# Performance work log

Hardware: AMD Instinct MI355X
Metric: run time of the kernel (lower is better)

Reference implementation:

```python
import jax, jax.numpy as jnp
import numpy as np
from jax import lax

SCORE_TH = 0.05
IOU_TH = 0.5
MAX_DET = 100  # fixed keep budget per class (torch version is variable-length; we pad)
BBOX_STD = jnp.array([0.1, 0.1, 0.2, 0.2], dtype=jnp.float32)


def setup_inputs() -> dict:
    key = jax.random.key(0)
    k1, k2, k3, k4 = jax.random.split(key, 4)
    A, C, H, W = 200000, 80, 768, 768
    # sigmoid-like scores, skewed low so the 0.05 threshold is meaningful
    classification = jax.random.uniform(k1, (A, C), dtype=jnp.float32) ** 4
    regression = jax.random.normal(k2, (A, 4), dtype=jnp.float32)
    ctr = jax.random.uniform(k3, (A, 2), dtype=jnp.float32, minval=0.0, maxval=float(W))
    wh = jax.random.uniform(k4, (A, 2), dtype=jnp.float32, minval=8.0, maxval=128.0)
    anchors = jnp.concatenate([ctr - 0.5 * wh, ctr + 0.5 * wh], axis=-1)  # valid x1y1x2y2
    return {"classification": classification, "regression": regression,
            "anchors": anchors, "img_h": H, "img_w": W}


def _decode_clip(anchors, regression, img_h, img_w):
    # BBoxTransform: RetinaNet delta decode with std [0.1,0.1,0.2,0.2], then ClipBoxes
    wa = anchors[:, 2] - anchors[:, 0]
    ha = anchors[:, 3] - anchors[:, 1]
    cxa = anchors[:, 0] + 0.5 * wa
    cya = anchors[:, 1] + 0.5 * ha
    d = regression * BBOX_STD
    cx = cxa + d[:, 0] * wa
    cy = cya + d[:, 1] * ha
    w = jnp.exp(d[:, 2]) * wa
    h = jnp.exp(d[:, 3]) * ha
    boxes = jnp.stack([cx - 0.5 * w, cy - 0.5 * h, cx + 0.5 * w, cy + 0.5 * h], axis=-1)
    lim = jnp.array([img_w, img_h, img_w, img_h], dtype=boxes.dtype)
    return jnp.clip(boxes, 0.0, lim)


def _nms_one(scores_c, boxes, areas):
    # greedy NMS for one class over all A anchors; fixed MAX_DET iterations
    s0 = jnp.where(scores_c > SCORE_TH, scores_c, -1.0)

    def step(s, _):
        i = jnp.argmax(s)
        valid = s[i] > 0.0
        b = boxes[i]
        xx1 = jnp.maximum(b[0], boxes[:, 0])
        yy1 = jnp.maximum(b[1], boxes[:, 1])
        xx2 = jnp.minimum(b[2], boxes[:, 2])
        yy2 = jnp.minimum(b[3], boxes[:, 3])
        inter = jnp.maximum(xx2 - xx1, 0.0) * jnp.maximum(yy2 - yy1, 0.0)
        iou = inter / (areas[i] + areas - inter)
        supp = (iou > IOU_TH) & valid
        s = jnp.where(supp, -1.0, s).at[i].set(-1.0)
        return s, (i, valid)

    _, (idx, val) = lax.scan(step, s0, None, length=MAX_DET)
    return idx, val  # [MAX_DET] int, [MAX_DET] bool


def _forward(classification, regression, anchors, img_h, img_w):
    boxes = _decode_clip(anchors, regression, img_h, img_w)  # [A,4]
    # NMS index selection is non-differentiable (as in torch); stop_gradient the selection path
    boxes_ng = lax.stop_gradient(boxes)
    scores_ng = lax.stop_gradient(classification)
    areas = (boxes_ng[:, 2] - boxes_ng[:, 0]) * (boxes_ng[:, 3] - boxes_ng[:, 1])
    idx, val = jax.vmap(_nms_one, in_axes=(1, None, None))(scores_ng, boxes_ng, areas)  # [C,M]
    C = classification.shape[1]
    sel_scores = jnp.take_along_axis(classification.T, idx, axis=1) * val          # [C,M]
    sel_boxes = boxes[idx] * val[..., None]                                        # [C,M,4]
    class_ids = jnp.where(val, jnp.arange(C, dtype=jnp.int32)[:, None], -1)        # [C,M]
    # torch returns variable-length concatenations; we return fixed-size padded
    # equivalents (invalid slots: score=0, class=-1, box=0)
    return sel_scores.reshape(-1), class_ids.reshape(-1), sel_boxes.reshape(-1, 4)


def reference(classification, regression, anchors, img_h, img_w):
    return _forward(classification, regression, anchors, img_h, img_w)
```

## Files before the change

### kernel.cpp

```cpp
#include <hip/hip_runtime.h>
#include <float.h>
#include <math.h>

#define SCORE_TH 0.05f
#define IOU_TH   0.5f
#define MAXD     100
#define CAP      512
#define HI_TH    0.996f
#define SWALK    192
#define NWORDS   3
#define CNT_STRIDE 16

__device__ __forceinline__ float4 decode_box(float4 an, float4 r, float W, float H)
{
    float wa = an.z - an.x, ha = an.w - an.y;
    float cxa = an.x + 0.5f * wa, cya = an.y + 0.5f * ha;
    float cx = cxa + r.x * 0.1f * wa;
    float cy = cya + r.y * 0.1f * ha;
    float w  = expf(r.z * 0.2f) * wa;
    float h  = expf(r.w * 0.2f) * ha;
    float x1 = cx - 0.5f * w, y1 = cy - 0.5f * h;
    float x2 = cx + 0.5f * w, y2 = cy + 0.5f * h;
    x1 = fminf(fmaxf(x1, 0.f), W);
    y1 = fminf(fmaxf(y1, 0.f), H);
    x2 = fminf(fmaxf(x2, 0.f), W);
    y2 = fminf(fmaxf(y2, 0.f), H);
    return make_float4(x1, y1, x2, y2);
}

template<int CC>
__global__ __launch_bounds__(256)
void k_compact(const float4* __restrict__ cls4, float2* __restrict__ cand,
               int* __restrict__ cnt, int* __restrict__ loflag,
               int C_rt, int total4)
{
    const int C = CC ? CC : C_rt;
    __shared__ unsigned char lflag[256];
    for (int i = threadIdx.x; i < C; i += blockDim.x) lflag[i] = 0;
    __syncthreads();

    const int gstride = gridDim.x * blockDim.x;
    const int gtid = blockIdx.x * blockDim.x + threadIdx.x;

    for (int j0 = gtid; j0 < total4; j0 += 4 * gstride) {
        int j1 = j0 + gstride, j2 = j0 + 2 * gstride, j3 = j0 + 3 * gstride;
        bool ok1 = j1 < total4, ok2 = j2 < total4, ok3 = j3 < total4;
        float4 v0 = cls4[j0];
        float4 v1 = ok1 ? cls4[j1] : make_float4(0.f, 0.f, 0.f, 0.f);
        float4 v2 = ok2 ? cls4[j2] : make_float4(0.f, 0.f, 0.f, 0.f);
        float4 v3 = ok3 ? cls4[j3] : make_float4(0.f, 0.f, 0.f, 0.f);

        #pragma unroll
        for (int w = 0; w < 4; w++) {
            float4 v = (w == 0) ? v0 : (w == 1) ? v1 : (w == 2) ? v2 : v3;
            if (w == 1 && !ok1) break;
            if (w == 2 && !ok2) break;
            if (w == 3 && !ok3) break;
            unsigned b = (unsigned)(j0 + w * gstride) * 4u;
            int c = (int)(b % (unsigned)C);
            int a = (int)(b / (unsigned)C);
            float s[4] = {v.x, v.y, v.z, v.w};
            #pragma unroll
            for (int j = 0; j < 4; j++) {
                float sc = s[j];
                if (sc > HI_TH) {
                    int pos = atomicAdd(&cnt[c * CNT_STRIDE], 1);
                    if (pos < CAP) cand[(size_t)c * CAP + pos] = make_float2(sc, __int_as_float(a));
                } else if (sc > SCORE_TH) {
                    lflag[c] = 1;
                }
                c++; if (c == C) { c = 0; a++; }
            }
        }
    }
    __syncthreads();
    for (int i = threadIdx.x; i < C; i += blockDim.x)
        if (lflag[i]) loflag[i] = 1;
}

__global__ __launch_bounds__(256)
void k_nms(const float4* __restrict__ anch, const float4* __restrict__ reg,
           const int* __restrict__ ph, const int* __restrict__ pw,
           const float2* __restrict__ cand, const int* __restrict__ cnt,
           const int* __restrict__ loflag, int* __restrict__ incomp,
           float* __restrict__ out, int C)
{
    int c = blockIdx.x;
    __shared__ unsigned long long keys[CAP];
    __shared__ float bx1[SWALK], by1[SWALK], bx2[SWALK], by2[SWALK], sar[SWALK];
    __shared__ unsigned long long mask[SWALK][NWORDS];
    __shared__ int kidx[MAXD];

    int n_raw = cnt[c * CNT_STRIDE];
    if (n_raw > CAP) {
        if (threadIdx.x == 0) incomp[c] = 1;
        return;
    }
    int n = n_raw;

    for (int i = threadIdx.x; i < CAP; i += blockDim.x) {
        if (i < n) {
            float2 e = cand[(size_t)c * CAP + i];
            unsigned sbits = __float_as_uint(e.x);
            unsigned aid   = (unsigned)__float_as_int(e.y);
            keys[i] = ((unsigned long long)(~sbits) << 32) | (unsigned long long)aid;
        } else {
            keys[i] = 0xFFFFFFFFFFFFFFFFull;
        }
    }
    __syncthreads();

    const int SORTN = (n <= 256) ? 256 : CAP;
    for (int k = 2; k <= SORTN; k <<= 1) {
        for (int j = k >> 1; j > 0; j >>= 1) {
            for (int i = threadIdx.x; i < SORTN; i += blockDim.x) {
                int ixj = i ^ j;
                if (ixj > i) {
                    unsigned long long a = keys[i], b = keys[ixj];
                    bool sw = ((i & k) == 0) ? (a > b) : (a < b);
                    if (sw) { keys[i] = b; keys[ixj] = a; }
                }
            }
            __syncthreads();
        }
    }

    float W = (float)(*pw), H = (float)(*ph);
    int nS = n < SWALK ? n : SWALK;
    for (int i = threadIdx.x; i < nS; i += blockDim.x) {
        unsigned aid = (unsigned)keys[i];
        float4 b = decode_box(anch[aid], reg[aid], W, H);
        bx1[i] = b.x; by1[i] = b.y; bx2[i] = b.z; by2[i] = b.w;
        sar[i] = (b.z - b.x) * (b.w - b.y);
    }
    __syncthreads();

    for (int task = threadIdx.x; task < nS * NWORDS; task += blockDim.x) {
        int i = task / NWORDS;
        int w = task - i * NWORDS;
        unsigned long long m = 0ull;
        int j0 = w << 6;
        int jend = j0 + 64 < nS ? j0 + 64 : nS;
        int js = j0 > i + 1 ? j0 : i + 1;
        float ix1 = bx1[i], iy1 = by1[i], ix2 = bx2[i], iy2 = by2[i], ia = sar[i];
        for (int j = js; j < jend; ++j) {
            float xx1 = fmaxf(ix1, bx1[j]);
            float yy1 = fmaxf(iy1, by1[j]);
            float xx2 = fminf(ix2, bx2[j]);
            float yy2 = fminf(iy2, by2[j]);
            float inter = fmaxf(xx2 - xx1, 0.f) * fmaxf(yy2 - yy1, 0.f);
            float iou = inter / (ia + sar[j] - inter);
            if (iou > IOU_TH) m |= 1ull << (j - j0);
        }
        mask[i][w] = m;
    }
    __syncthreads();

    unsigned long long rem0 = 0, rem1 = 0, rem2 = 0;
    int kept = 0;
    for (int k = 0; k < nS && kept < MAXD; ++k) {
        unsigned long long m0 = mask[k][0], m1 = mask[k][1], m2 = mask[k][2];
        unsigned long long rw = (k < 64) ? rem0 : (k < 128) ? rem1 : rem2;
        if (!((rw >> (k & 63)) & 1ull)) {
            if (threadIdx.x == 0) kidx[kept] = k;
            ++kept;
            rem0 |= m0; rem1 |= m1; rem2 |= m2;
        }
    }
    __syncthreads();

    if (kept < MAXD && (n > nS || loflag[c] != 0)) {
        if (threadIdx.x == 0) incomp[c] = 1;
        return;
    }

    int total = C * MAXD;
    int base = c * MAXD;
    for (int m = threadIdx.x; m < kept; m += blockDim.x) {
        int k = kidx[m];
        unsigned long long key = keys[k];
        float sc = __uint_as_float(~(unsigned)(key >> 32));
        out[base + m] = sc;
        out[total + base + m] = (float)c;
        float* ob = out + 2 * (size_t)total + (size_t)(base + m) * 4;
        ob[0] = bx1[k]; ob[1] = by1[k]; ob[2] = bx2[k]; ob[3] = by2[k];
    }
    for (int m = kept + threadIdx.x; m < MAXD; m += blockDim.x) {
        out[base + m] = 0.f;
        out[total + base + m] = -1.f;
        float* ob = out + 2 * (size_t)total + (size_t)(base + m) * 4;
        ob[0] = 0.f; ob[1] = 0.f; ob[2] = 0.f; ob[3] = 0.f;
    }
}

__global__ __launch_bounds__(256)
void k_fallback(const float* __restrict__ cls,
                const float4* __restrict__ anch, const float4* __restrict__ reg,
                const int* __restrict__ ph, const int* __restrict__ pw,
                const int* __restrict__ incomp, float* __restrict__ out,
                int A, int C)
{
    int c = blockIdx.x;
    if (!incomp[c]) return;
    __shared__ float kx1[MAXD], ky1[MAXD], kx2[MAXD], ky2[MAXD], kar[MAXD];
    __shared__ float rs[4]; __shared__ int ra[4];
    __shared__ float cs; __shared__ int caid; __shared__ int have; __shared__ int suppflag;
    int lane = threadIdx.x & 63, wid = threadIdx.x >> 6;
    float W = (float)(*pw), H = (float)(*ph);
    float s_last = FLT_MAX; int a_last = -1;
    int kept = 0;
    int total = C * MAXD;
    for (long long guard = 0; guard <= (long long)A && kept < MAXD; guard++) {
        float bs = -1.f; int ba = 0x7fffffff;
        for (int a = threadIdx.x; a < A; a += blockDim.x) {
            float s = cls[(size_t)a * C + c];
            if (s <= SCORE_TH) continue;
            if (s > s_last || (s == s_last && a <= a_last)) continue;
            if (s > bs || (s == bs && a < ba)) { bs = s; ba = a; }
        }
        for (int off = 32; off >= 1; off >>= 1) {
            float s2 = __shfl_down(bs, off);
            int a2 = __shfl_down(ba, off);
            if (s2 > bs || (s2 == bs && a2 < ba)) { bs = s2; ba = a2; }
        }
        if (lane == 0) { rs[wid] = bs; ra[wid] = ba; }
        __syncthreads();
        if (threadIdx.x == 0) {
            float fs = rs[0]; int fa = ra[0];
            for (int w = 1; w < 4; w++)
                if (rs[w] > fs || (rs[w] == fs && ra[w] < fa)) { fs = rs[w]; fa = ra[w]; }
            cs = fs; caid = fa; have = (fs > 0.f) ? 1 : 0;
        }
        __syncthreads();
        if (!have) break;
        float s_c = cs; int a_c = caid;
        s_last = s_c; a_last = a_c;
        float4 b = decode_box(anch[a_c], reg[a_c], W, H);
        float ar = (b.z - b.x) * (b.w - b.y);
        if (threadIdx.x == 0) suppflag = 0;
        __syncthreads();
        for (int k = threadIdx.x; k < kept; k += blockDim.x) {
            float xx1 = fmaxf(b.x, kx1[k]);
            float yy1 = fmaxf(b.y, ky1[k]);
            float xx2 = fminf(b.z, kx2[k]);
            float yy2 = fminf(b.w, ky2[k]);
            float inter = fmaxf(xx2 - xx1, 0.f) * fmaxf(yy2 - yy1, 0.f);
            float iou = inter / (ar + kar[k] - inter);
            if (iou > IOU_TH) suppflag = 1;
        }
        __syncthreads();
        if (!suppflag) {
            if (threadIdx.x == 0) {
                kx1[kept] = b.x; ky1[kept] = b.y; kx2[kept] = b.z; ky2[kept] = b.w; kar[kept] = ar;
                int slot = c * MAXD + kept;
                out[slot] = s_c;
                out[total + slot] = (float)c;
                float* ob = out + 2 * (size_t)total + (size_t)slot * 4;
                ob[0] = b.x; ob[1] = b.y; ob[2] = b.z; ob[3] = b.w;
            }
            kept++;
        }
        __syncthreads();
    }
    for (int k = kept + threadIdx.x; k < MAXD; k += blockDim.x) {
        int slot = c * MAXD + k;
        out[slot] = 0.f;
        out[total + slot] = -1.f;
        float* ob = out + 2 * (size_t)total + (size_t)slot * 4;
        ob[0] = 0.f; ob[1] = 0.f; ob[2] = 0.f; ob[3] = 0.f;
    }
}

extern "C" void kernel_launch(void* const* d_in, const int* in_sizes, int n_in,
                              void* d_out, int out_size, void* d_ws, size_t ws_size,
                              hipStream_t stream)
{
    const float*  cls  = (const float*)d_in[0];
    const float4* reg  = (const float4*)d_in[1];
    const float4* anch = (const float4*)d_in[2];
    const int*    ph   = (const int*)d_in[3];
    const int*    pw   = (const int*)d_in[4];
    int A = in_sizes[1] / 4;
    int C = in_sizes[0] / A;
    float* out = (float*)d_out;

    char* ws = (char*)d_ws;
    float2* cand = (float2*)ws;
    int* ctrl   = (int*)(cand + (size_t)C * CAP);
    int* cnt    = ctrl;
    int* loflag = ctrl + C * CNT_STRIDE;
    int* incomp = loflag + C;

    hipMemsetAsync(ctrl, 0, (C * CNT_STRIDE + 2 * C) * sizeof(int), stream);

    int total4 = (int)((long long)A * C / 4);
    int blocks2 = (total4 + 255) / 256;
    if (blocks2 > 2048) blocks2 = 2048;
    if (C == 80 && (long long)A * C < (1LL << 31))
        k_compact<80><<<blocks2, 256, 0, stream>>>((const float4*)cls, cand, cnt, loflag, C, total4);
    else
        k_compact<0><<<blocks2, 256, 0, stream>>>((const float4*)cls, cand, cnt, loflag, C, total4);

    k_nms<<<C, 256, 0, stream>>>(anch, reg, ph, pw, cand, cnt, loflag, incomp, out, C);
    k_fallback<<<C, 256, 0, stream>>>(cls, anch, reg, ph, pw, incomp, out, A, C);
}
```

Baseline: 145.9 us.

## Inline fallback NMS into main kernel and batch greedy mask walk

Removes the separate fallback kernel launch by calling the slow-path class NMS inline from k_nms when a class overflows or is incomplete, dropping the incomp flag array and shrinking the memset. Splits the suppression mask into three per-word arrays so the greedy walk can load four rows at a time with vector loads and accept four unsuppressed, non-suppressing candidates in one step. Also limits key initialisation to the sort size. It saves a launch and some serial walk work, but adds shared memory and code size to k_nms, which may lower occupancy.

```diff
diff --git a/kernel.cpp b/kernel.cpp
--- a/kernel.cpp
+++ b/kernel.cpp
@@ -78,27 +78,103 @@
         if (lflag[i]) loflag[i] = 1;
 }
 
+__device__ void fallback_class(const float* __restrict__ cls,
+                               const float4* __restrict__ anch, const float4* __restrict__ reg,
+                               float W, float H, int A, int C, int c,
+                               float* __restrict__ out)
+{
+    __shared__ float kx1[MAXD], ky1[MAXD], kx2[MAXD], ky2[MAXD], kar[MAXD];
+    __shared__ float rs[4]; __shared__ int ra[4];
+    __shared__ float cs; __shared__ int caid; __shared__ int have; __shared__ int suppflag;
+    int lane = threadIdx.x & 63, wid = threadIdx.x >> 6;
+    float s_last = FLT_MAX; int a_last = -1;
+    int kept = 0;
+    int total = C * MAXD;
+    for (long long guard = 0; guard <= (long long)A && kept < MAXD; guard++) {
+        float bs = -1.f; int ba = 0x7fffffff;
+        for (int a = threadIdx.x; a < A; a += blockDim.x) {
+            float s = cls[(size_t)a * C + c];
+            if (s <= SCORE_TH) continue;
+            if (s > s_last || (s == s_last && a <= a_last)) continue;
+            if (s > bs || (s == bs && a < ba)) { bs = s; ba = a; }
+        }
+        for (int off = 32; off >= 1; off >>= 1) {
+            float s2 = __shfl_down(bs, off);
+            int a2 = __shfl_down(ba, off);
+            if (s2 > bs || (s2 == bs && a2 < ba)) { bs = s2; ba = a2; }
+        }
+        if (lane == 0) { rs[wid] = bs; ra[wid] = ba; }
+        __syncthreads();
+        if (threadIdx.x == 0) {
+            float fs = rs[0]; int fa = ra[0];
+            for (int w = 1; w < 4; w++)
+                if (rs[w] > fs || (rs[w] == fs && ra[w] < fa)) { fs = rs[w]; fa = ra[w]; }
+            cs = fs; caid = fa; have = (fs > 0.f) ? 1 : 0;
+        }
+        __syncthreads();
+        if (!have) break;
+        float s_c = cs; int a_c = caid;
+        s_last = s_c; a_last = a_c;
+        float4 b = decode_box(anch[a_c], reg[a_c], W, H);
+        float ar = (b.z - b.x) * (b.w - b.y);
+        if (threadIdx.x == 0) suppflag = 0;
+        __syncthreads();
+        for (int k = threadIdx.x; k < kept; k += blockDim.x) {
+            float xx1 = fmaxf(b.x, kx1[k]);
+            float yy1 = fmaxf(b.y, ky1[k]);
+            float xx2 = fminf(b.z, kx2[k]);
+            float yy2 = fminf(b.w, ky2[k]);
+            float inter = fmaxf(xx2 - xx1, 0.f) * fmaxf(yy2 - yy1, 0.f);
+            float iou = inter / (ar + kar[k] - inter);
+            if (iou > IOU_TH) suppflag = 1;
+        }
+        __syncthreads();
+        if (!suppflag) {
+            if (threadIdx.x == 0) {
+                kx1[kept] = b.x; ky1[kept] = b.y; kx2[kept] = b.z; ky2[kept] = b.w; kar[kept] = ar;
+                int slot = c * MAXD + kept;
+                out[slot] = s_c;
+                out[total + slot] = (float)c;
+                float* ob = out + 2 * (size_t)total + (size_t)slot * 4;
+                ob[0] = b.x; ob[1] = b.y; ob[2] = b.z; ob[3] = b.w;
+            }
+            kept++;
+        }
+        __syncthreads();
+    }
+    for (int k = kept + threadIdx.x; k < MAXD; k += blockDim.x) {
+        int slot = c * MAXD + k;
+        out[slot] = 0.f;
+        out[total + slot] = -1.f;
+        float* ob = out + 2 * (size_t)total + (size_t)slot * 4;
+        ob[0] = 0.f; ob[1] = 0.f; ob[2] = 0.f; ob[3] = 0.f;
+    }
+}
+
 __global__ __launch_bounds__(256)
-void k_nms(const float4* __restrict__ anch, const float4* __restrict__ reg,
+void k_nms(const float* __restrict__ cls,
+           const float4* __restrict__ anch, const float4* __restrict__ reg,
            const int* __restrict__ ph, const int* __restrict__ pw,
            const float2* __restrict__ cand, const int* __restrict__ cnt,
-           const int* __restrict__ loflag, int* __restrict__ incomp,
-           float* __restrict__ out, int C)
+           const int* __restrict__ loflag,
+           float* __restrict__ out, int A, int C)
 {
     int c = blockIdx.x;
     __shared__ unsigned long long keys[CAP];
     __shared__ float bx1[SWALK], by1[SWALK], bx2[SWALK], by2[SWALK], sar[SWALK];
-    __shared__ unsigned long long mask[SWALK][NWORDS];
+    __shared__ __align__(16) unsigned long long m0[SWALK], m1[SWALK], m2[SWALK];
     __shared__ int kidx[MAXD];
 
+    float W = (float)(*pw), H = (float)(*ph);
     int n_raw = cnt[c * CNT_STRIDE];
     if (n_raw > CAP) {
-        if (threadIdx.x == 0) incomp[c] = 1;
+        fallback_class(cls, anch, reg, W, H, A, C, c, out);
         return;
     }
     int n = n_raw;
 
-    for (int i = threadIdx.x; i < CAP; i += blockDim.x) {
+    const int SORTN = (n <= 256) ? 256 : CAP;
+    for (int i = threadIdx.x; i < SORTN; i += blockDim.x) {
         if (i < n) {
             float2 e = cand[(size_t)c * CAP + i];
             unsigned sbits = __float_as_uint(e.x);
@@ -110,7 +186,6 @@
     }
     __syncthreads();
 
-    const int SORTN = (n <= 256) ? 256 : CAP;
     for (int k = 2; k <= SORTN; k <<= 1) {
         for (int j = k >> 1; j > 0; j >>= 1) {
             for (int i = threadIdx.x; i < SORTN; i += blockDim.x) {
@@ -125,7 +200,6 @@
         }
     }
 
-    float W = (float)(*pw), H = (float)(*ph);
     int nS = n < SWALK ? n : SWALK;
     for (int i = threadIdx.x; i < nS; i += blockDim.x) {
         unsigned aid = (unsigned)keys[i];
@@ -152,25 +226,50 @@
             float iou = inter / (ia + sar[j] - inter);
             if (iou > IOU_TH) m |= 1ull << (j - j0);
         }
-        mask[i][w] = m;
+        if (w == 0) m0[i] = m; else if (w == 1) m1[i] = m; else m2[i] = m;
     }
     __syncthreads();
 
     unsigned long long rem0 = 0, rem1 = 0, rem2 = 0;
     int kept = 0;
-    for (int k = 0; k < nS && kept < MAXD; ++k) {
-        unsigned long long m0 = mask[k][0], m1 = mask[k][1], m2 = mask[k][2];
-        unsigned long long rw = (k < 64) ? rem0 : (k < 128) ? rem1 : rem2;
-        if (!((rw >> (k & 63)) & 1ull)) {
-            if (threadIdx.x == 0) kidx[kept] = k;
-            ++kept;
-            rem0 |= m0; rem1 |= m1; rem2 |= m2;
+    for (int k0 = 0; k0 < nS && kept < MAXD; k0 += 4) {
+        ulonglong2 A0 = *(const ulonglong2*)&m0[k0];
+        ulonglong2 A1 = *(const ulonglong2*)&m0[k0 + 2];
+        ulonglong2 B0 = *(const ulonglong2*)&m1[k0];
+        ulonglong2 B1 = *(const ulonglong2*)&m1[k0 + 2];
+        ulonglong2 C0 = *(const ulonglong2*)&m2[k0];
+        ulonglong2 C1 = *(const ulonglong2*)&m2[k0 + 2];
+        unsigned long long g = A0.x | A0.y | A1.x | A1.y | B0.x | B0.y | B1.x | B1.y
+                             | C0.x | C0.y | C1.x | C1.y;
+        unsigned long long rw4 = ((k0 < 64) ? rem0 : (k0 < 128) ? rem1 : rem2) >> (k0 & 63);
+        if (g == 0ull && (rw4 & 0xFull) == 0ull && k0 + 4 <= nS && kept + 4 <= MAXD) {
+            if (threadIdx.x == 0) {
+                kidx[kept] = k0; kidx[kept + 1] = k0 + 1;
+                kidx[kept + 2] = k0 + 2; kidx[kept + 3] = k0 + 3;
+            }
+            kept += 4;
+            continue;
+        }
+        #pragma unroll
+        for (int s = 0; s < 4; ++s) {
+            int k = k0 + s;
+            if (k < nS && kept < MAXD) {
+                unsigned long long mm0 = (s == 0) ? A0.x : (s == 1) ? A0.y : (s == 2) ? A1.x : A1.y;
+                unsigned long long mm1 = (s == 0) ? B0.x : (s == 1) ? B0.y : (s == 2) ? B1.x : B1.y;
+                unsigned long long mm2 = (s == 0) ? C0.x : (s == 1) ? C0.y : (s == 2) ? C1.x : C1.y;
+                unsigned long long rw = (k < 64) ? rem0 : (k < 128) ? rem1 : rem2;
+                if (!((rw >> (k & 63)) & 1ull)) {
+                    if (threadIdx.x == 0) kidx[kept] = k;
+                    ++kept;
+                    rem0 |= mm0; rem1 |= mm1; rem2 |= mm2;
+                }
+            }
         }
     }
     __syncthreads();
 
     if (kept < MAXD && (n > nS || loflag[c] != 0)) {
-        if (threadIdx.x == 0) incomp[c] = 1;
+        fallback_class(cls, anch, reg, W, H, A, C, c, out);
         return;
     }
 
@@ -193,84 +292,6 @@
     }
 }
 
-__global__ __launch_bounds__(256)
-void k_fallback(const float* __restrict__ cls,
-                const float4* __restrict__ anch, const float4* __restrict__ reg,
-                const int* __restrict__ ph, const int* __restrict__ pw,
-                const int* __restrict__ incomp, float* __restrict__ out,
-                int A, int C)
-{
-    int c = blockIdx.x;
-    if (!incomp[c]) return;
-    __shared__ float kx1[MAXD], ky1[MAXD], kx2[MAXD], ky2[MAXD], kar[MAXD];
-    __shared__ float rs[4]; __shared__ int ra[4];
-    __shared__ float cs; __shared__ int caid; __shared__ int have; __shared__ int suppflag;
-    int lane = threadIdx.x & 63, wid = threadIdx.x >> 6;
-    float W = (float)(*pw), H = (float)(*ph);
-    float s_last = FLT_MAX; int a_last = -1;
-    int kept = 0;
-    int total = C * MAXD;
-    for (long long guard = 0; guard <= (long long)A && kept < MAXD; guard++) {
-        float bs = -1.f; int ba = 0x7fffffff;
-        for (int a = threadIdx.x; a < A; a += blockDim.x) {
-            float s = cls[(size_t)a * C + c];
-            if (s <= SCORE_TH) continue;
-            if (s > s_last || (s == s_last && a <= a_last)) continue;
-            if (s > bs || (s == bs && a < ba)) { bs = s; ba = a; }
-        }
-        for (int off = 32; off >= 1; off >>= 1) {
-            float s2 = __shfl_down(bs, off);
-            int a2 = __shfl_down(ba, off);
-            if (s2 > bs || (s2 == bs && a2 < ba)) { bs = s2; ba = a2; }
-        }
-        if (lane == 0) { rs[wid] = bs; ra[wid] = ba; }
-        __syncthreads();
-        if (threadIdx.x == 0) {
-            float fs = rs[0]; int fa = ra[0];
-            for (int w = 1; w < 4; w++)
-                if (rs[w] > fs || (rs[w] == fs && ra[w] < fa)) { fs = rs[w]; fa = ra[w]; }
-            cs = fs; caid = fa; have = (fs > 0.f) ? 1 : 0;
-        }
-        __syncthreads();
-        if (!have) break;
-        float s_c = cs; int a_c = caid;
-        s_last = s_c; a_last = a_c;
-        float4 b = decode_box(anch[a_c], reg[a_c], W, H);
-        float ar = (b.z - b.x) * (b.w - b.y);
-        if (threadIdx.x == 0) suppflag = 0;
-        __syncthreads();
-        for (int k = threadIdx.x; k < kept; k += blockDim.x) {
-            float xx1 = fmaxf(b.x, kx1[k]);
-            float yy1 = fmaxf(b.y, ky1[k]);
-            float xx2 = fminf(b.z, kx2[k]);
-            float yy2 = fminf(b.w, ky2[k]);
-            float inter = fmaxf(xx2 - xx1, 0.f) * fmaxf(yy2 - yy1, 0.f);
-            float iou = inter / (ar + kar[k] - inter);
-            if (iou > IOU_TH) suppflag = 1;
-        }
-        __syncthreads();
-        if (!suppflag) {
-            if (threadIdx.x == 0) {
-                kx1[kept] = b.x; ky1[kept] = b.y; kx2[kept] = b.z; ky2[kept] = b.w; kar[kept] = ar;
-                int slot = c * MAXD + kept;
-                out[slot] = s_c;
-                out[total + slot] = (float)c;
-                float* ob = out + 2 * (size_t)total + (size_t)slot * 4;
-                ob[0] = b.x; ob[1] = b.y; ob[2] = b.z; ob[3] = b.w;
-            }
-            kept++;
-        }
-        __syncthreads();
-    }
-    for (int k = kept + threadIdx.x; k < MAXD; k += blockDim.x) {
-        int slot = c * MAXD + k;
-        out[slot] = 0.f;
-        out[total + slot] = -1.f;
-        float* ob = out + 2 * (size_t)total + (size_t)slot * 4;
-        ob[0] = 0.f; ob[1] = 0.f; ob[2] = 0.f; ob[3] = 0.f;
-    }
-}
-
 extern "C" void kernel_launch(void* const* d_in, const int* in_sizes, int n_in,
                               void* d_out, int out_size, void* d_ws, size_t ws_size,
                               hipStream_t stream)
@@ -289,9 +310,8 @@
     int* ctrl   = (int*)(cand + (size_t)C * CAP);
     int* cnt    = ctrl;
     int* loflag = ctrl + C * CNT_STRIDE;
-    int* incomp = loflag + C;
-
-    hipMemsetAsync(ctrl, 0, (C * CNT_STRIDE + 2 * C) * sizeof(int), stream);
+
+    hipMemsetAsync(ctrl, 0, (C * CNT_STRIDE + C) * sizeof(int), stream);
 
     int total4 = (int)((long long)A * C / 4);
     int blocks2 = (total4 + 255) / 256;
@@ -301,6 +321,5 @@
     else
         k_compact<0><<<blocks2, 256, 0, stream>>>((const float4*)cls, cand, cnt, loflag, C, total4);
 
-    k_nms<<<C, 256, 0, stream>>>(anch, reg, ph, pw, cand, cnt, loflag, incomp, out, C);
-    k_fallback<<<C, 256, 0, stream>>>(cls, anch, reg, ph, pw, incomp, out, A, C);
-}
+    k_nms<<<C, 256, 0, stream>>>(cls, anch, reg, ph, pw, cand, cnt, loflag, out, A, C);
+}
```

Result: faster. 140.3 us (-3.8%).
